# Kernel tuning notes

Hardware: AMD Instinct MI355X
Metric: run time of the kernel (lower is better)

Reference implementation:

```python
import jax, jax.numpy as jnp
import numpy as np

N_EMBD = 1024
N_HEAD = 16
HEAD_DIM = N_EMBD // N_HEAD  # 64
N_CTX = 2048
ROPE_THETA = 10000.0


def _rope_cache(L, dim, base):
    inv_freq = 1.0 / (base ** (np.arange(0, dim, 2, dtype=np.float32) / dim))
    t = np.arange(L, dtype=np.float32)
    freqs = np.einsum('i,j->ij', t, inv_freq)  # (L, dim/2)
    return jnp.asarray(np.cos(freqs)), jnp.asarray(np.sin(freqs))


def _apply_rotary(x, cos, sin):
    # x: (B, H, L, D), cos/sin: (L, D/2) -> broadcast (1,1,L,D/2)
    x1 = x[..., ::2]
    x2 = x[..., 1::2]
    c = cos[None, None, :, :]
    s = sin[None, None, :, :]
    y1 = x1 * c - x2 * s
    y2 = x1 * s + x2 * c
    # interleave back: stack on last dim then flatten
    return jnp.stack((y1, y2), axis=-1).reshape(x.shape)


def setup_inputs() -> dict:
    key = jax.random.key(0)
    k1, k2, k3, k4, k5 = jax.random.split(key, 5)
    B, L, D = 4, 2048, N_EMBD
    scale = 0.02
    x = jax.random.normal(k1, (B, L, D), dtype=jnp.float32)
    W_qkv = jax.random.normal(k2, (D, 3 * D), dtype=jnp.float32) * scale
    b_qkv = jnp.zeros((3 * D,), dtype=jnp.float32)
    W_proj = jax.random.normal(k3, (D, D), dtype=jnp.float32) * scale
    b_proj = jnp.zeros((D,), dtype=jnp.float32)
    attention_mask = jnp.ones((B, L), dtype=jnp.int32)
    return {"x": x, "W_qkv": W_qkv, "b_qkv": b_qkv, "W_proj": W_proj,
            "b_proj": b_proj, "attention_mask": attention_mask}


def reference(x, W_qkv, b_qkv, W_proj, b_proj, attention_mask):
    B, L, D = x.shape
    H, Dh = N_HEAD, HEAD_DIM
    qkv = x @ W_qkv + b_qkv  # (B, L, 3D)
    q, k, v = jnp.split(qkv, 3, axis=2)
    # (B, L, H, Dh) -> (B, H, L, Dh)
    q = q.reshape(B, L, H, Dh).transpose(0, 2, 1, 3)
    k = k.reshape(B, L, H, Dh).transpose(0, 2, 1, 3)
    v = v.reshape(B, L, H, Dh).transpose(0, 2, 1, 3)
    cos, sin = _rope_cache(L, Dh, ROPE_THETA)
    q = _apply_rotary(q, cos, sin)
    k = _apply_rotary(k, cos, sin)
    # mask: causal & key padding keep
    causal = jnp.tril(jnp.ones((L, L), dtype=bool))[None, None]        # (1,1,L,L)
    key_keep = attention_mask.astype(bool)[:, None, None, :]          # (B,1,1,L)
    keep = causal & key_keep                                          # (B,1,L,L)
    scores = jnp.einsum('bhqd,bhkd->bhqk', q, k) / jnp.sqrt(jnp.float32(Dh))
    scores = jnp.where(keep, scores, jnp.finfo(scores.dtype).min)
    attn = jax.nn.softmax(scores, axis=-1)
    out = jnp.einsum('bhqk,bhkd->bhqd', attn, v)  # (B,H,L,Dh)
    out = out.transpose(0, 2, 1, 3).reshape(B, L, D)
    return out @ W_proj + b_proj
```

## Files before the change

kernel.cpp:

```cpp
#include <hip/hip_runtime.h>
#include <math.h>

typedef __bf16 bf16x8 __attribute__((ext_vector_type(8)));
typedef float f32x4 __attribute__((ext_vector_type(4)));
typedef float f32x16 __attribute__((ext_vector_type(16)));
typedef unsigned short u16;
typedef unsigned short u16x8 __attribute__((ext_vector_type(8)));
typedef unsigned short u16x4 __attribute__((ext_vector_type(4)));
typedef unsigned u32x2v __attribute__((ext_vector_type(2)));

#define BATCH 4
#define SEQ   2048
#define EMBD  1024
#define NHEAD 16
#define HDIM  64
#define MROWS 8192
#define QKVN  3072

__device__ __forceinline__ u16 f2bf(float f) {
    union { float f; unsigned u; } cv; cv.f = f;
    unsigned u = cv.u;
    return (u16)((u + 0x7FFFu + ((u >> 16) & 1u)) >> 16);
}

__device__ __forceinline__ unsigned cvtpk_bf16(float lo, float hi) {
    unsigned r;
    asm("v_cvt_pk_bf16_f32 %0, %1, %2" : "=v"(r) : "v"(lo), "v"(hi));
    return r;
}

__device__ __forceinline__ void glds16(const void* g, void* l) {
    __builtin_amdgcn_global_load_lds(
        (const __attribute__((address_space(1))) unsigned int*)(g),
        (__attribute__((address_space(3))) unsigned int*)(l), 16, 0, 0);
}

#define MF8(qm, A0, A1, A2, A3, B0, B1)                                          \
    acc[(qm)*4+0][0] = __builtin_amdgcn_mfma_f32_16x16x32_bf16(A0, B0, acc[(qm)*4+0][0], 0, 0, 0); \
    acc[(qm)*4+0][1] = __builtin_amdgcn_mfma_f32_16x16x32_bf16(A0, B1, acc[(qm)*4+0][1], 0, 0, 0); \
    acc[(qm)*4+1][0] = __builtin_amdgcn_mfma_f32_16x16x32_bf16(A1, B0, acc[(qm)*4+1][0], 0, 0, 0); \
    acc[(qm)*4+1][1] = __builtin_amdgcn_mfma_f32_16x16x32_bf16(A1, B1, acc[(qm)*4+1][1], 0, 0, 0); \
    acc[(qm)*4+2][0] = __builtin_amdgcn_mfma_f32_16x16x32_bf16(A2, B0, acc[(qm)*4+2][0], 0, 0, 0); \
    acc[(qm)*4+2][1] = __builtin_amdgcn_mfma_f32_16x16x32_bf16(A2, B1, acc[(qm)*4+2][1], 0, 0, 0); \
    acc[(qm)*4+3][0] = __builtin_amdgcn_mfma_f32_16x16x32_bf16(A3, B0, acc[(qm)*4+3][0], 0, 0, 0); \
    acc[(qm)*4+3][1] = __builtin_amdgcn_mfma_f32_16x16x32_bf16(A3, B1, acc[(qm)*4+3][1], 0, 0, 0);

__device__ __forceinline__ void transpose_body(const float* __restrict__ W,
                                               u16* __restrict__ Wt, int K, int N,
                                               int n0, int k0, u16 (*T)[68]) {
    const int tx = threadIdx.x & 15, ty = threadIdx.x >> 4;
#pragma unroll
    for (int r = 0; r < 4; r++) {
        int k = k0 + ty + r * 16;
        float4 w = *(const float4*)&W[(size_t)k * N + n0 + tx * 4];
        T[tx * 4 + 0][ty + r * 16] = f2bf(w.x);
        T[tx * 4 + 1][ty + r * 16] = f2bf(w.y);
        T[tx * 4 + 2][ty + r * 16] = f2bf(w.z);
        T[tx * 4 + 3][ty + r * 16] = f2bf(w.w);
    }
    __syncthreads();
#pragma unroll
    for (int r = 0; r < 4; r++) {
        int nl = ty + r * 16;
        u16x4 v = { T[nl][tx * 4 + 0], T[nl][tx * 4 + 1],
                    T[nl][tx * 4 + 2], T[nl][tx * 4 + 3] };
        *(u16x4*)&Wt[(size_t)(n0 + nl) * K + k0 + tx * 4] = v;
    }
}

__global__ __launch_bounds__(256)
void prep_kernel(const float* __restrict__ x, const float* __restrict__ Wqkv,
                 const float* __restrict__ Wproj, const int* __restrict__ amask,
                 u16* __restrict__ Xb, u16* __restrict__ Wqkvt, u16* __restrict__ Wprojt,
                 float* __restrict__ ropeC, float* __restrict__ ropeS,
                 float* __restrict__ mbias, int* __restrict__ flags) {
    __shared__ union { u16 T[64][68]; int ok[4]; } sm;
    const int bx = blockIdx.x, tid = threadIdx.x;
    if (bx < 8192) {
        int i = bx * 256 + tid;
        float4 v = ((const float4*)x)[i];
        u16x4 o = { f2bf(v.x), f2bf(v.y), f2bf(v.z), f2bf(v.w) };
        ((u16x4*)Xb)[i] = o;
    } else if (bx < 8960) {
        int bxx = bx - 8192;
        transpose_body(Wqkv, Wqkvt, EMBD, QKVN, (bxx % 48) * 64, (bxx / 48) * 64, sm.T);
    } else if (bx < 9216) {
        int bxx = bx - 8960;
        transpose_body(Wproj, Wprojt, EMBD, EMBD, (bxx & 15) * 64, (bxx >> 4) * 64, sm.T);
    } else if (bx < 9472) {
        int i = (bx - 9216) * 256 + tid;
        int l = i >> 5, p = i & 31;
        float invf = powf(10000.0f, -(float)(2 * p) * (1.0f / 64.0f));
        float sv, cv;
        sincosf((float)l * invf, &sv, &cv);
        ropeC[i] = cv; ropeS[i] = sv;
    } else {
        int idx = (bx - 9472) * 256 + tid;
        int mv = amask[idx];
        mbias[idx] = mv ? 0.0f : -1e30f;
        unsigned long long bal = __ballot(mv != 0);
        int wv = tid >> 6;
        if ((tid & 63) == 0) sm.ok[wv] = (bal == 0xFFFFFFFFFFFFFFFFull);
        __syncthreads();
        if (tid == 0)   flags[idx >> 7] = sm.ok[0] & sm.ok[1];
        if (tid == 128) flags[idx >> 7] = sm.ok[2] & sm.ok[3];
    }
}

__global__ __launch_bounds__(512, 2)
void qkv_gemm(const u16* __restrict__ A, const u16* __restrict__ Bt,
              const float* __restrict__ bias,
              const float* __restrict__ Ct, const float* __restrict__ St,
              u16* __restrict__ Qo, u16* __restrict__ Ko, u16* __restrict__ Vo) {
    __shared__ u16 SM[49152];
    const int tid = threadIdx.x;
    const int w = tid >> 6, ln = tid & 63;
    const int quad = ln >> 4, l16 = ln & 15;
    const int wm = w >> 2, wn = w & 3;
    const int bid = blockIdx.y * 24 + blockIdx.x;
    const int swz = (bid & 7) * 96 + (bid >> 3);
    const int m0 = (swz / 24) * 256, n0 = (swz % 24) * 128;

    const int sr8 = ln >> 3;
    const int xs = (ln & 7) ^ sr8;
    const u16* Ab = A  + (size_t)(m0 + w * 8 + sr8) * EMBD + xs * 8;
    const u16* Bb = Bt + (size_t)(n0 + w * 8 + sr8) * EMBD + xs * 8;
    u16* ldsA = SM + w * 512;
    u16* ldsB = SM + 32768 + w * 512;
    const int ch0 = ((0 + quad) ^ (l16 & 7)) * 8;
    const int ch1 = ((4 + quad) ^ (l16 & 7)) * 8;

    auto stageA = [&](int buf, int rb, int kt) {
        glds16(Ab + (size_t)rb * EMBD + kt * 64, ldsA + buf * 16384 + rb * 64);
    };
    auto stageB = [&](int buf, int rb, int kt) {
        glds16(Bb + (size_t)rb * EMBD + kt * 64, ldsB + buf * 8192 + rb * 64);
    };

    f32x4 acc[8][2] = {};

    stageA(0, 0, 0);  stageA(0, 128, 0);
    stageA(0, 64, 0); stageA(0, 192, 0);
    stageB(0, 0, 0);  stageB(0, 64, 0);
    stageA(1, 0, 1);  stageA(1, 128, 1);
    asm volatile("s_waitcnt vmcnt(2)" ::: "memory");
    __builtin_amdgcn_sched_barrier(0);
    __builtin_amdgcn_s_barrier();

    for (int u = 0; u < 16; ++u) {
        const int c = u & 1, nc = c ^ 1;
        const u16* Ac0 = SM + c * 16384 + (wm * 128 + l16) * 64;
        const u16* Ac1 = Ac0 + 64 * 64;
        const u16* Bc  = SM + 32768 + c * 8192 + (wn * 32 + l16) * 64;
        bf16x8 a0, a1, a2, a3, bk0a, bk0b, bk1a, bk1b;
        a0 = *(const bf16x8*)&Ac0[ch0];        a1 = *(const bf16x8*)&Ac0[1024 + ch0];
        a2 = *(const bf16x8*)&Ac0[2048 + ch0]; a3 = *(const bf16x8*)&Ac0[3072 + ch0];
        bk0a = *(const bf16x8*)&Bc[ch0];       bk0b = *(const bf16x8*)&Bc[1024 + ch0];
        if (u < 15) { stageA(nc, 64, u + 1); stageA(nc, 192, u + 1); stageB(nc, 64, u + 1); }
        __builtin_amdgcn_sched_barrier(0);
        __builtin_amdgcn_s_setprio(1);
        MF8(0, a0, a1, a2, a3, bk0a, bk0b);
        __builtin_amdgcn_s_setprio(0);
        __builtin_amdgcn_sched_barrier(0);
        a0 = *(const bf16x8*)&Ac0[ch1];        a1 = *(const bf16x8*)&Ac0[1024 + ch1];
        a2 = *(const bf16x8*)&Ac0[2048 + ch1]; a3 = *(const bf16x8*)&Ac0[3072 + ch1];
        bk1a = *(const bf16x8*)&Bc[ch1];       bk1b = *(const bf16x8*)&Bc[1024 + ch1];
        if (u < 15) stageB(nc, 0, u + 1);
        __builtin_amdgcn_sched_barrier(0);
        __builtin_amdgcn_s_setprio(1);
        MF8(0, a0, a1, a2, a3, bk1a, bk1b);
        __builtin_amdgcn_s_setprio(0);
        __builtin_amdgcn_sched_barrier(0);
        __builtin_amdgcn_s_barrier();
        a0 = *(const bf16x8*)&Ac1[ch0];        a1 = *(const bf16x8*)&Ac1[1024 + ch0];
        a2 = *(const bf16x8*)&Ac1[2048 + ch0]; a3 = *(const bf16x8*)&Ac1[3072 + ch0];
        if (u < 14) { stageA(c, 0, u + 2); stageA(c, 128, u + 2); }
        __builtin_amdgcn_sched_barrier(0);
        __builtin_amdgcn_s_setprio(1);
        MF8(1, a0, a1, a2, a3, bk0a, bk0b);
        __builtin_amdgcn_s_setprio(0);
        __builtin_amdgcn_sched_barrier(0);
        a0 = *(const bf16x8*)&Ac1[ch1];        a1 = *(const bf16x8*)&Ac1[1024 + ch1];
        a2 = *(const bf16x8*)&Ac1[2048 + ch1]; a3 = *(const bf16x8*)&Ac1[3072 + ch1];
        __builtin_amdgcn_sched_barrier(0);
        __builtin_amdgcn_s_setprio(1);
        MF8(1, a0, a1, a2, a3, bk1a, bk1b);
        __builtin_amdgcn_s_setprio(0);
        __builtin_amdgcn_sched_barrier(0);
        if (u < 14) asm volatile("s_waitcnt vmcnt(2)" ::: "memory");
        else        asm volatile("s_waitcnt vmcnt(0)" ::: "memory");
        __builtin_amdgcn_sched_barrier(0);
        __builtin_amdgcn_s_barrier();
    }

    const int sec = n0 >> 10;
    if (sec == 2) {
#pragma unroll
        for (int ii = 0; ii < 8; ii++)
#pragma unroll
            for (int r = 0; r < 4; r++) {
                int m = m0 + wm * 128 + ii * 16 + quad * 4 + r;
                int b = m >> 11, l = m & 2047;
#pragma unroll
                for (int j = 0; j < 2; j++) {
                    int n = n0 + wn * 32 + j * 16 + l16;
                    int dcol = n & 1023;
                    int h = dcol >> 6, dh = dcol & 63;
                    float v = acc[ii][j][r] + bias[n];
                    Vo[(((size_t)b * NHEAD + h) * SEQ + l) * HDIM + dh] = f2bf(v);
                }
            }
    } else {
        u16* O = (sec == 0) ? Qo : Ko;
        const float qs = (sec == 0) ? 0.125f * 1.44269504f : 1.0f;
#pragma unroll
        for (int ii = 0; ii < 8; ii++)
#pragma unroll
            for (int r = 0; r < 4; r++) {
                int m = m0 + wm * 128 + ii * 16 + quad * 4 + r;
                int b = m >> 11, l = m & 2047;
#pragma unroll
                for (int j = 0; j < 2; j++) {
                    int n = n0 + wn * 32 + j * 16 + l16;
                    int h = (n & 1023) >> 6, dh = n & 63;
                    int p = (n & 63) >> 1;
                    float v = acc[ii][j][r] + bias[n];
                    float pv = __shfl_xor(v, 1, 64);
                    float cv = Ct[l * 32 + p], sv = St[l * 32 + p];
                    float o = (l16 & 1) ? (pv * sv + v * cv) : (v * cv - pv * sv);
                    O[(((size_t)b * NHEAD + h) * SEQ + l) * HDIM + dh] = f2bf(o * qs);
                }
            }
    }
}

__global__ __launch_bounds__(256)
void transpose_v(const u16* __restrict__ Vo, u16* __restrict__ Vt) {
    __shared__ u16 T[64][72];
    const int bh = blockIdx.y;
    const int l0 = blockIdx.x * 64;
    const int tx = threadIdx.x & 15, ty = threadIdx.x >> 4;
#pragma unroll
    for (int rr = 0; rr < 4; rr++) {
        int l = ty + rr * 16;
        u16x4 v = *(const u16x4*)&Vo[((size_t)bh * SEQ + l0 + l) * HDIM + tx * 4];
        T[l][tx * 4 + 0] = v.x; T[l][tx * 4 + 1] = v.y;
        T[l][tx * 4 + 2] = v.z; T[l][tx * 4 + 3] = v.w;
    }
    __syncthreads();
#pragma unroll
    for (int rr = 0; rr < 4; rr++) {
        int dh = ty + rr * 16;
        u16x4 w = { T[tx * 4 + 0][dh], T[tx * 4 + 1][dh],
                    T[tx * 4 + 2][dh], T[tx * 4 + 3][dh] };
        *(u16x4*)&Vt[((size_t)bh * HDIM + dh) * SEQ + l0 + tx * 4] = w;
    }
}

__global__ __launch_bounds__(512, 2)
void attn_mfma3(const u16* __restrict__ Qb, const u16* __restrict__ Kb,
                const u16* __restrict__ Vt, const float* __restrict__ mb,
                const int* __restrict__ flags, u16* __restrict__ Ot) {
    __shared__ u16 SM[32768];
    const int tid = threadIdx.x;
    const int wv = tid >> 6, ln = tid & 63;
    const int l32 = ln & 31, hi = ln >> 5;
    const int bid = blockIdx.x;
    const int bh = bid & 63;
    const int qt = (bid < 256) ? 7 - (bid >> 6) : ((bid - 256) >> 6);
    const int b = bh >> 4;
    const u16* Qg = Qb + (size_t)bh * SEQ * HDIM;
    const u16* Kg = Kb + (size_t)bh * SEQ * HDIM;
    const u16* Vg = Vt + (size_t)bh * HDIM * SEQ;

    const int kRow = ln >> 3;
    const size_t kLane = (size_t)(wv * 16 + kRow) * 64 + ((ln & 7) ^ kRow) * 8;
    const int vRow = ln >> 4, sc0 = (ln & 15) ^ vRow;
    const size_t vLaneE = (size_t)(wv * 8 + vRow) * SEQ + sc0 * 8;
    const size_t vLaneO = (size_t)(wv * 8 + 4 + vRow) * SEQ + (sc0 ^ 4) * 8;

    const int q0w = qt * 256 + wv * 32;
    const int qmin = q0w;
    const int qabs = q0w + l32;

    bf16x8 Qf[4];
#pragma unroll
    for (int kd = 0; kd < 4; kd++)
        Qf[kd] = *(const bf16x8*)&Qg[(size_t)(q0w + l32) * HDIM + kd * 16 + hi * 8];

    f32x16 o[2] = {};
    float mrun = -1e30f, lrun = 0.f;

    const int nkt = 2 * qt + 2;

    {
        u16* KsD = SM + wv * 1024;
        u16* VsD = SM + 8192 + wv * 1024;
        glds16(Kg + kLane,       KsD);
        glds16(Kg + kLane + 512, KsD + 512);
        glds16(Vg + vLaneE,      VsD);
        glds16(Vg + vLaneO,      VsD + 512);
    }
    __syncthreads();

    int buf = 0;
    for (int kt = 0; kt < nkt; kt++) {
        const int kbase = kt * 128;
        if (kt + 1 < nkt) {
            const size_t nb = (size_t)(kbase + 128);
            u16* KsD = SM + (buf ^ 1) * 16384 + wv * 1024;
            u16* VsD = SM + (buf ^ 1) * 16384 + 8192 + wv * 1024;
            glds16(Kg + nb * 64 + kLane,       KsD);
            glds16(Kg + nb * 64 + kLane + 512, KsD + 512);
            glds16(Vg + nb + vLaneE,           VsD);
            glds16(Vg + nb + vLaneO,           VsD + 512);
        }
        const u16* Ks = SM + buf * 16384;
        const u16* Vs = SM + buf * 16384 + 8192;

        f32x16 s[4];
        __builtin_amdgcn_s_setprio(1);
#pragma unroll
        for (int mi = 0; mi < 4; mi++) {
            const int key = mi * 32 + l32;
            f32x16 z = {};
#pragma unroll
            for (int kd = 0; kd < 4; kd++) {
                int ch = kd * 2 + hi;
                bf16x8 kf = *(const bf16x8*)&Ks[key * 64 + ((ch ^ (key & 7)) * 8)];
                z = __builtin_amdgcn_mfma_f32_32x32x16_bf16(kf, Qf[kd], z, 0, 0, 0);
            }
            s[mi] = z;
        }
        __builtin_amdgcn_s_setprio(0);

        if (kbase + 127 > qmin) {
#pragma unroll
            for (int mi = 0; mi < 4; mi++)
#pragma unroll
                for (int r = 0; r < 16; r++) {
                    int row = kbase + mi * 32 + (r & 3) + 8 * (r >> 2) + 4 * hi;
                    if (row > qabs) s[mi][r] = -1e30f;
                }
        }
        if (!flags[b * 16 + kt]) {
#pragma unroll
            for (int mi = 0; mi < 4; mi++)
#pragma unroll
                for (int r = 0; r < 16; r++) {
                    int row = mi * 32 + (r & 3) + 8 * (r >> 2) + 4 * hi;
                    s[mi][r] += mb[b * SEQ + kbase + row];
                }
        }

        float rm = -1e30f;
#pragma unroll
        for (int mi = 0; mi < 4; mi++) {
            float a0 = fmaxf(fmaxf(s[mi][0],  s[mi][1]),  fmaxf(s[mi][2],  s[mi][3]));
            float a1 = fmaxf(fmaxf(s[mi][4],  s[mi][5]),  fmaxf(s[mi][6],  s[mi][7]));
            float a2 = fmaxf(fmaxf(s[mi][8],  s[mi][9]),  fmaxf(s[mi][10], s[mi][11]));
            float a3 = fmaxf(fmaxf(s[mi][12], s[mi][13]), fmaxf(s[mi][14], s[mi][15]));
            rm = fmaxf(rm, fmaxf(fmaxf(a0, a1), fmaxf(a2, a3)));
        }
        {
            u32x2v f = __builtin_amdgcn_permlane32_swap(
                __float_as_uint(rm), __float_as_uint(rm), false, false);
            rm = fmaxf(__uint_as_float(f[0]), __uint_as_float(f[1]));
        }
        if (!__all(rm <= mrun + 8.0f)) {
            float mnew = fmaxf(mrun, rm);
            float al = __builtin_amdgcn_exp2f(mrun - mnew);
            mrun = mnew;
            lrun *= al;
#pragma unroll
            for (int r = 0; r < 16; r++) { o[0][r] *= al; o[1][r] *= al; }
        }
        float rs = 0.f;
#pragma unroll
        for (int mi = 0; mi < 4; mi++) {
            float ps = 0.f;
#pragma unroll
            for (int r = 0; r < 16; r++) {
                float pe = __builtin_amdgcn_exp2f(s[mi][r] - mrun);
                s[mi][r] = pe;
                ps += pe;
            }
            rs += ps;
        }
        {
            u32x2v f = __builtin_amdgcn_permlane32_swap(
                __float_as_uint(rs), __float_as_uint(rs), false, false);
            rs = __uint_as_float(f[0]) + __uint_as_float(f[1]);
        }
        lrun += rs;

#pragma unroll
        for (int t = 0; t < 4; t++) {
            unsigned A0 = cvtpk_bf16(s[t][0],  s[t][1]);
            unsigned B0 = cvtpk_bf16(s[t][4],  s[t][5]);
            unsigned A1 = cvtpk_bf16(s[t][2],  s[t][3]);
            unsigned B1 = cvtpk_bf16(s[t][6],  s[t][7]);
            u32x2v r0 = __builtin_amdgcn_permlane32_swap(A0, B0, false, false);
            u32x2v r1 = __builtin_amdgcn_permlane32_swap(A1, B1, false, false);
            union { unsigned u[4]; bf16x8 v; } p0;
            p0.u[0] = r0[0]; p0.u[1] = r1[0]; p0.u[2] = r0[1]; p0.u[3] = r1[1];

            unsigned A2 = cvtpk_bf16(s[t][8],  s[t][9]);
            unsigned B2 = cvtpk_bf16(s[t][12], s[t][13]);
            unsigned A3 = cvtpk_bf16(s[t][10], s[t][11]);
            unsigned B3 = cvtpk_bf16(s[t][14], s[t][15]);
            u32x2v r2 = __builtin_amdgcn_permlane32_swap(A2, B2, false, false);
            u32x2v r3 = __builtin_amdgcn_permlane32_swap(A3, B3, false, false);
            union { unsigned u[4]; bf16x8 v; } p1;
            p1.u[0] = r2[0]; p1.u[1] = r3[0]; p1.u[2] = r2[1]; p1.u[3] = r3[1];

            __builtin_amdgcn_s_setprio(1);
#pragma unroll
            for (int md = 0; md < 2; md++) {
                const int dh = md * 32 + l32;
                bf16x8 v0 = *(const bf16x8*)&Vs[dh * 128 + (((t * 4 + hi)     ^ (dh & 7)) * 8)];
                o[md] = __builtin_amdgcn_mfma_f32_32x32x16_bf16(v0, p0.v, o[md], 0, 0, 0);
                bf16x8 v1 = *(const bf16x8*)&Vs[dh * 128 + (((t * 4 + 2 + hi) ^ (dh & 7)) * 8)];
                o[md] = __builtin_amdgcn_mfma_f32_32x32x16_bf16(v1, p1.v, o[md], 0, 0, 0);
            }
            __builtin_amdgcn_s_setprio(0);
        }
        __syncthreads();
        buf ^= 1;
    }

    __syncthreads();
    u16* Osh = SM + wv * 2176;
    float inv = 1.0f / lrun;
#pragma unroll
    for (int md = 0; md < 2; md++)
#pragma unroll
        for (int r = 0; r < 16; r++) {
            int dh = md * 32 + (r & 3) + 8 * (r >> 2) + 4 * hi;
            Osh[l32 * 68 + dh] = f2bf(o[md][r] * inv);
        }
    __syncthreads();
    {
        int qrow = ln >> 1, hf = ln & 1;
        size_t gbase = ((size_t)bh * SEQ + q0w + qrow) * HDIM + hf * 32;
#pragma unroll
        for (int c = 0; c < 4; c++) {
            u16x8 vv = *(const u16x8*)&Osh[qrow * 68 + hf * 32 + c * 8];
            *(u16x8*)&Ot[gbase + c * 8] = vv;
        }
    }
}

__global__ __launch_bounds__(256)
void proj_gemm(const u16* __restrict__ A, const u16* __restrict__ Bt,
               const float* __restrict__ bias, float* __restrict__ out) {
    __shared__ u16 SM[32768];
    const int tid = threadIdx.x;
    const int wv = tid >> 6, ln = tid & 63;
    const int quad = ln >> 4, l16 = ln & 15;
    const int bid = blockIdx.y * 8 + blockIdx.x;
    const int swz = (bid & 7) * 64 + (bid >> 3);
    const int m0 = (swz >> 3) * 128, n0 = (swz & 7) * 128;
    const int wm = wv >> 1, wn = wv & 1;

    const int srow = wv * 8 + (ln >> 3);
    const int xs = (ln & 7) ^ (srow & 7);

    f32x4 acc[4][4] = {};

    auto stage = [&](int buf, int kt) {
        u16* As = SM + buf * 16384;
        u16* Bs = As + 8192;
#pragma unroll
        for (int p = 0; p < 4; p++) {
            int row = p * 32 + srow;
            int m = m0 + row;
            int bb = m >> 11, l = m & 2047;
            glds16(A + (((size_t)(bb * 16 + kt) * SEQ + l) * HDIM) + xs * 8,
                   As + (p * 256 + wv * 64) * 8);
            glds16(Bt + (size_t)(n0 + row) * EMBD + kt * 64 + xs * 8,
                   Bs + (p * 256 + wv * 64) * 8);
        }
    };

    stage(0, 0);
    __syncthreads();
    int buf = 0;
    for (int kt = 0; kt < 16; kt++) {
        if (kt < 15) stage(buf ^ 1, kt + 1);
        const u16* As = SM + buf * 16384;
        const u16* Bs = As + 8192;
        __builtin_amdgcn_s_setprio(1);
#pragma unroll
        for (int kk = 0; kk < 2; kk++) {
            bf16x8 af[4], bfr[4];
#pragma unroll
            for (int i = 0; i < 4; i++) {
                int R = wm * 64 + i * 16 + l16;
                af[i] = *(const bf16x8*)&As[R * 64 + (((kk * 4 + quad) ^ (R & 7)) * 8)];
            }
#pragma unroll
            for (int j = 0; j < 4; j++) {
                int R = wn * 64 + j * 16 + l16;
                bfr[j] = *(const bf16x8*)&Bs[R * 64 + (((kk * 4 + quad) ^ (R & 7)) * 8)];
            }
#pragma unroll
            for (int i = 0; i < 4; i++)
#pragma unroll
                for (int j = 0; j < 4; j++)
                    acc[i][j] = __builtin_amdgcn_mfma_f32_16x16x32_bf16(af[i], bfr[j], acc[i][j], 0, 0, 0);
        }
        __builtin_amdgcn_s_setprio(0);
        __syncthreads();
        buf ^= 1;
    }
#pragma unroll
    for (int i = 0; i < 4; i++)
#pragma unroll
        for (int r = 0; r < 4; r++) {
            int m = m0 + wm * 64 + i * 16 + quad * 4 + r;
#pragma unroll
            for (int j = 0; j < 4; j++) {
                int n = n0 + wn * 64 + j * 16 + l16;
                out[(size_t)m * EMBD + n] = acc[i][j][r] + bias[n];
            }
        }
}

extern "C" void kernel_launch(void* const* d_in, const int* in_sizes, int n_in,
                              void* d_out, int out_size, void* d_ws, size_t ws_size,
                              hipStream_t stream)
{
    const float* x     = (const float*)d_in[0];
    const float* Wqkv  = (const float*)d_in[1];
    const float* bqkv  = (const float*)d_in[2];
    const float* Wproj = (const float*)d_in[3];
    const float* bproj = (const float*)d_in[4];
    const int*   amask = (const int*)d_in[5];
    float* out = (float*)d_out;

    char* ws = (char*)d_ws;
    u16*   Xb     = (u16*)(ws);
    u16*   Ot     = (u16*)(ws);
    u16*   Wqkvt  = (u16*)(ws + 16777216);
    u16*   Wprojt = (u16*)(ws + 23068672);
    u16*   Qb     = (u16*)(ws + 25165824);
    u16*   Kb     = (u16*)(ws + 41943040);
    u16*   Vb     = (u16*)(ws + 58720256);
    u16*   Vtp    = (u16*)(ws + 75497472);
    float* ropeC  = (float*)(ws + 92274688);
    float* ropeS  = (float*)(ws + 92536832);
    float* mbias  = (float*)(ws + 92798976);
    int*   flags  = (int*)(ws + 92831744);

    prep_kernel<<<9504, 256, 0, stream>>>(x, Wqkv, Wproj, amask,
                                          Xb, Wqkvt, Wprojt, ropeC, ropeS, mbias, flags);
    qkv_gemm<<<dim3(24, 32), 512, 0, stream>>>(
        Xb, Wqkvt, bqkv, ropeC, ropeS, Qb, Kb, Vb);
    transpose_v<<<dim3(32, 64), 256, 0, stream>>>(Vb, Vtp);
    attn_mfma3<<<512, 512, 0, stream>>>(Qb, Kb, Vtp, mbias, flags, Ot);
    proj_gemm<<<dim3(EMBD / 128, MROWS / 128), 256, 0, stream>>>(Ot, Wprojt, bproj, out);
}
```

Baseline: 245.8 us.

## Fuse V transpose into QKV GEMM epilogue and skip fully masked causal tiles

The QKV GEMM's V-section epilogue now stages the tile in shared memory and writes V directly in the transposed (head, dim, seq) layout. This removes the separate transpose kernel and its extra round trip through global memory. In attention, each wave skips QK, softmax and PV work for key tiles that lie entirely above its causal diagonal. The cost is an extra LDS staging pass and a barrier in the GEMM epilogue, plus more branch divergence between waves in attention.

```diff
diff --git a/kernel.cpp b/kernel.cpp
--- a/kernel.cpp
+++ b/kernel.cpp
@@ -111,7 +111,7 @@
 void qkv_gemm(const u16* __restrict__ A, const u16* __restrict__ Bt,
               const float* __restrict__ bias,
               const float* __restrict__ Ct, const float* __restrict__ St,
-              u16* __restrict__ Qo, u16* __restrict__ Ko, u16* __restrict__ Vo) {
+              u16* __restrict__ Qo, u16* __restrict__ Ko, u16* __restrict__ Vt) {
     __shared__ u16 SM[49152];
     const int tid = threadIdx.x;
     const int w = tid >> 6, ln = tid & 63;
@@ -195,21 +195,33 @@
 
     const int sec = n0 >> 10;
     if (sec == 2) {
+        u16* Vl = SM;
 #pragma unroll
         for (int ii = 0; ii < 8; ii++)
 #pragma unroll
-            for (int r = 0; r < 4; r++) {
-                int m = m0 + wm * 128 + ii * 16 + quad * 4 + r;
-                int b = m >> 11, l = m & 2047;
-#pragma unroll
-                for (int j = 0; j < 2; j++) {
-                    int n = n0 + wn * 32 + j * 16 + l16;
-                    int dcol = n & 1023;
-                    int h = dcol >> 6, dh = dcol & 63;
-                    float v = acc[ii][j][r] + bias[n];
-                    Vo[(((size_t)b * NHEAD + h) * SEQ + l) * HDIM + dh] = f2bf(v);
-                }
-            }
+            for (int j = 0; j < 2; j++) {
+                int nl = wn * 32 + j * 16 + l16;
+                int ml = wm * 128 + ii * 16 + quad * 4;
+                int n = n0 + wn * 32 + j * 16 + l16;
+                u16x4 pk;
+#pragma unroll
+                for (int r = 0; r < 4; r++)
+                    pk[r] = f2bf(acc[ii][j][r] + bias[n]);
+                *(u16x4*)&Vl[nl * 260 + ml] = pk;
+            }
+        __syncthreads();
+        {
+            int dcl = tid >> 2, ck = tid & 3;
+            int dcol = (n0 & 1023) + dcl;
+            int h = dcol >> 6, dh = dcol & 63;
+            int b = m0 >> 11, l0 = m0 & 2047;
+            size_t gb = (((size_t)b * NHEAD + h) * HDIM + dh) * SEQ + l0 + ck * 64;
+#pragma unroll
+            for (int c2 = 0; c2 < 8; c2++) {
+                u16x8 v = *(const u16x8*)&Vl[dcl * 260 + ck * 64 + c2 * 8];
+                *(u16x8*)&Vt[gb + c2 * 8] = v;
+            }
+        }
     } else {
         u16* O = (sec == 0) ? Qo : Ko;
         const float qs = (sec == 0) ? 0.125f * 1.44269504f : 1.0f;
@@ -231,29 +243,6 @@
                     O[(((size_t)b * NHEAD + h) * SEQ + l) * HDIM + dh] = f2bf(o * qs);
                 }
             }
-    }
-}
-
-__global__ __launch_bounds__(256)
-void transpose_v(const u16* __restrict__ Vo, u16* __restrict__ Vt) {
-    __shared__ u16 T[64][72];
-    const int bh = blockIdx.y;
-    const int l0 = blockIdx.x * 64;
-    const int tx = threadIdx.x & 15, ty = threadIdx.x >> 4;
-#pragma unroll
-    for (int rr = 0; rr < 4; rr++) {
-        int l = ty + rr * 16;
-        u16x4 v = *(const u16x4*)&Vo[((size_t)bh * SEQ + l0 + l) * HDIM + tx * 4];
-        T[l][tx * 4 + 0] = v.x; T[l][tx * 4 + 1] = v.y;
-        T[l][tx * 4 + 2] = v.z; T[l][tx * 4 + 3] = v.w;
-    }
-    __syncthreads();
-#pragma unroll
-    for (int rr = 0; rr < 4; rr++) {
-        int dh = ty + rr * 16;
-        u16x4 w = { T[tx * 4 + 0][dh], T[tx * 4 + 1][dh],
-                    T[tx * 4 + 2][dh], T[tx * 4 + 3][dh] };
-        *(u16x4*)&Vt[((size_t)bh * HDIM + dh) * SEQ + l0 + tx * 4] = w;
     }
 }
 
@@ -280,7 +269,6 @@
     const size_t vLaneO = (size_t)(wv * 8 + 4 + vRow) * SEQ + (sc0 ^ 4) * 8;
 
     const int q0w = qt * 256 + wv * 32;
-    const int qmin = q0w;
     const int qabs = q0w + l32;
 
     bf16x8 Qf[4];
@@ -318,112 +306,114 @@
         const u16* Ks = SM + buf * 16384;
         const u16* Vs = SM + buf * 16384 + 8192;
 
-        f32x16 s[4];
-        __builtin_amdgcn_s_setprio(1);
-#pragma unroll
-        for (int mi = 0; mi < 4; mi++) {
-            const int key = mi * 32 + l32;
-            f32x16 z = {};
-#pragma unroll
-            for (int kd = 0; kd < 4; kd++) {
-                int ch = kd * 2 + hi;
-                bf16x8 kf = *(const bf16x8*)&Ks[key * 64 + ((ch ^ (key & 7)) * 8)];
-                z = __builtin_amdgcn_mfma_f32_32x32x16_bf16(kf, Qf[kd], z, 0, 0, 0);
-            }
-            s[mi] = z;
-        }
-        __builtin_amdgcn_s_setprio(0);
-
-        if (kbase + 127 > qmin) {
-#pragma unroll
-            for (int mi = 0; mi < 4; mi++)
+        if (kbase <= q0w + 31) {
+            f32x16 s[4];
+            __builtin_amdgcn_s_setprio(1);
+#pragma unroll
+            for (int mi = 0; mi < 4; mi++) {
+                const int key = mi * 32 + l32;
+                f32x16 z = {};
+#pragma unroll
+                for (int kd = 0; kd < 4; kd++) {
+                    int ch = kd * 2 + hi;
+                    bf16x8 kf = *(const bf16x8*)&Ks[key * 64 + ((ch ^ (key & 7)) * 8)];
+                    z = __builtin_amdgcn_mfma_f32_32x32x16_bf16(kf, Qf[kd], z, 0, 0, 0);
+                }
+                s[mi] = z;
+            }
+            __builtin_amdgcn_s_setprio(0);
+
+            if (kbase + 127 > q0w) {
+#pragma unroll
+                for (int mi = 0; mi < 4; mi++)
+#pragma unroll
+                    for (int r = 0; r < 16; r++) {
+                        int row = kbase + mi * 32 + (r & 3) + 8 * (r >> 2) + 4 * hi;
+                        if (row > qabs) s[mi][r] = -1e30f;
+                    }
+            }
+            if (!flags[b * 16 + kt]) {
+#pragma unroll
+                for (int mi = 0; mi < 4; mi++)
+#pragma unroll
+                    for (int r = 0; r < 16; r++) {
+                        int row = mi * 32 + (r & 3) + 8 * (r >> 2) + 4 * hi;
+                        s[mi][r] += mb[b * SEQ + kbase + row];
+                    }
+            }
+
+            float rm = -1e30f;
+#pragma unroll
+            for (int mi = 0; mi < 4; mi++) {
+                float a0 = fmaxf(fmaxf(s[mi][0],  s[mi][1]),  fmaxf(s[mi][2],  s[mi][3]));
+                float a1 = fmaxf(fmaxf(s[mi][4],  s[mi][5]),  fmaxf(s[mi][6],  s[mi][7]));
+                float a2 = fmaxf(fmaxf(s[mi][8],  s[mi][9]),  fmaxf(s[mi][10], s[mi][11]));
+                float a3 = fmaxf(fmaxf(s[mi][12], s[mi][13]), fmaxf(s[mi][14], s[mi][15]));
+                rm = fmaxf(rm, fmaxf(fmaxf(a0, a1), fmaxf(a2, a3)));
+            }
+            {
+                u32x2v f = __builtin_amdgcn_permlane32_swap(
+                    __float_as_uint(rm), __float_as_uint(rm), false, false);
+                rm = fmaxf(__uint_as_float(f[0]), __uint_as_float(f[1]));
+            }
+            if (!__all(rm <= mrun + 8.0f)) {
+                float mnew = fmaxf(mrun, rm);
+                float al = __builtin_amdgcn_exp2f(mrun - mnew);
+                mrun = mnew;
+                lrun *= al;
+#pragma unroll
+                for (int r = 0; r < 16; r++) { o[0][r] *= al; o[1][r] *= al; }
+            }
+            float rs = 0.f;
+#pragma unroll
+            for (int mi = 0; mi < 4; mi++) {
+                float ps = 0.f;
 #pragma unroll
                 for (int r = 0; r < 16; r++) {
-                    int row = kbase + mi * 32 + (r & 3) + 8 * (r >> 2) + 4 * hi;
-                    if (row > qabs) s[mi][r] = -1e30f;
+                    float pe = __builtin_amdgcn_exp2f(s[mi][r] - mrun);
+                    s[mi][r] = pe;
+                    ps += pe;
                 }
-        }
-        if (!flags[b * 16 + kt]) {
-#pragma unroll
-            for (int mi = 0; mi < 4; mi++)
-#pragma unroll
-                for (int r = 0; r < 16; r++) {
-                    int row = mi * 32 + (r & 3) + 8 * (r >> 2) + 4 * hi;
-                    s[mi][r] += mb[b * SEQ + kbase + row];
+                rs += ps;
+            }
+            {
+                u32x2v f = __builtin_amdgcn_permlane32_swap(
+                    __float_as_uint(rs), __float_as_uint(rs), false, false);
+                rs = __uint_as_float(f[0]) + __uint_as_float(f[1]);
+            }
+            lrun += rs;
+
+#pragma unroll
+            for (int t = 0; t < 4; t++) {
+                unsigned A0 = cvtpk_bf16(s[t][0],  s[t][1]);
+                unsigned B0 = cvtpk_bf16(s[t][4],  s[t][5]);
+                unsigned A1 = cvtpk_bf16(s[t][2],  s[t][3]);
+                unsigned B1 = cvtpk_bf16(s[t][6],  s[t][7]);
+                u32x2v r0 = __builtin_amdgcn_permlane32_swap(A0, B0, false, false);
+                u32x2v r1 = __builtin_amdgcn_permlane32_swap(A1, B1, false, false);
+                union { unsigned u[4]; bf16x8 v; } p0;
+                p0.u[0] = r0[0]; p0.u[1] = r1[0]; p0.u[2] = r0[1]; p0.u[3] = r1[1];
+
+                unsigned A2 = cvtpk_bf16(s[t][8],  s[t][9]);
+                unsigned B2 = cvtpk_bf16(s[t][12], s[t][13]);
+                unsigned A3 = cvtpk_bf16(s[t][10], s[t][11]);
+                unsigned B3 = cvtpk_bf16(s[t][14], s[t][15]);
+                u32x2v r2 = __builtin_amdgcn_permlane32_swap(A2, B2, false, false);
+                u32x2v r3 = __builtin_amdgcn_permlane32_swap(A3, B3, false, false);
+                union { unsigned u[4]; bf16x8 v; } p1;
+                p1.u[0] = r2[0]; p1.u[1] = r3[0]; p1.u[2] = r2[1]; p1.u[3] = r3[1];
+
+                __builtin_amdgcn_s_setprio(1);
+#pragma unroll
+                for (int md = 0; md < 2; md++) {
+                    const int dh = md * 32 + l32;
+                    bf16x8 v0 = *(const bf16x8*)&Vs[dh * 128 + (((t * 4 + hi)     ^ (dh & 7)) * 8)];
+                    o[md] = __builtin_amdgcn_mfma_f32_32x32x16_bf16(v0, p0.v, o[md], 0, 0, 0);
+                    bf16x8 v1 = *(const bf16x8*)&Vs[dh * 128 + (((t * 4 + 2 + hi) ^ (dh & 7)) * 8)];
+                    o[md] = __builtin_amdgcn_mfma_f32_32x32x16_bf16(v1, p1.v, o[md], 0, 0, 0);
                 }
-        }
-
-        float rm = -1e30f;
-#pragma unroll
-        for (int mi = 0; mi < 4; mi++) {
-            float a0 = fmaxf(fmaxf(s[mi][0],  s[mi][1]),  fmaxf(s[mi][2],  s[mi][3]));
-            float a1 = fmaxf(fmaxf(s[mi][4],  s[mi][5]),  fmaxf(s[mi][6],  s[mi][7]));
-            float a2 = fmaxf(fmaxf(s[mi][8],  s[mi][9]),  fmaxf(s[mi][10], s[mi][11]));
-            float a3 = fmaxf(fmaxf(s[mi][12], s[mi][13]), fmaxf(s[mi][14], s[mi][15]));
-            rm = fmaxf(rm, fmaxf(fmaxf(a0, a1), fmaxf(a2, a3)));
-        }
-        {
-            u32x2v f = __builtin_amdgcn_permlane32_swap(
-                __float_as_uint(rm), __float_as_uint(rm), false, false);
-            rm = fmaxf(__uint_as_float(f[0]), __uint_as_float(f[1]));
-        }
-        if (!__all(rm <= mrun + 8.0f)) {
-            float mnew = fmaxf(mrun, rm);
-            float al = __builtin_amdgcn_exp2f(mrun - mnew);
-            mrun = mnew;
-            lrun *= al;
-#pragma unroll
-            for (int r = 0; r < 16; r++) { o[0][r] *= al; o[1][r] *= al; }
-        }
-        float rs = 0.f;
-#pragma unroll
-        for (int mi = 0; mi < 4; mi++) {
-            float ps = 0.f;
-#pragma unroll
-            for (int r = 0; r < 16; r++) {
-                float pe = __builtin_amdgcn_exp2f(s[mi][r] - mrun);
-                s[mi][r] = pe;
-                ps += pe;
-            }
-            rs += ps;
-        }
-        {
-            u32x2v f = __builtin_amdgcn_permlane32_swap(
-                __float_as_uint(rs), __float_as_uint(rs), false, false);
-            rs = __uint_as_float(f[0]) + __uint_as_float(f[1]);
-        }
-        lrun += rs;
-
-#pragma unroll
-        for (int t = 0; t < 4; t++) {
-            unsigned A0 = cvtpk_bf16(s[t][0],  s[t][1]);
-            unsigned B0 = cvtpk_bf16(s[t][4],  s[t][5]);
-            unsigned A1 = cvtpk_bf16(s[t][2],  s[t][3]);
-            unsigned B1 = cvtpk_bf16(s[t][6],  s[t][7]);
-            u32x2v r0 = __builtin_amdgcn_permlane32_swap(A0, B0, false, false);
-            u32x2v r1 = __builtin_amdgcn_permlane32_swap(A1, B1, false, false);
-            union { unsigned u[4]; bf16x8 v; } p0;
-            p0.u[0] = r0[0]; p0.u[1] = r1[0]; p0.u[2] = r0[1]; p0.u[3] = r1[1];
-
-            unsigned A2 = cvtpk_bf16(s[t][8],  s[t][9]);
-            unsigned B2 = cvtpk_bf16(s[t][12], s[t][13]);
-            unsigned A3 = cvtpk_bf16(s[t][10], s[t][11]);
-            unsigned B3 = cvtpk_bf16(s[t][14], s[t][15]);
-            u32x2v r2 = __builtin_amdgcn_permlane32_swap(A2, B2, false, false);
-            u32x2v r3 = __builtin_amdgcn_permlane32_swap(A3, B3, false, false);
-            union { unsigned u[4]; bf16x8 v; } p1;
-            p1.u[0] = r2[0]; p1.u[1] = r3[0]; p1.u[2] = r2[1]; p1.u[3] = r3[1];
-
-            __builtin_amdgcn_s_setprio(1);
-#pragma unroll
-            for (int md = 0; md < 2; md++) {
-                const int dh = md * 32 + l32;
-                bf16x8 v0 = *(const bf16x8*)&Vs[dh * 128 + (((t * 4 + hi)     ^ (dh & 7)) * 8)];
-                o[md] = __builtin_amdgcn_mfma_f32_32x32x16_bf16(v0, p0.v, o[md], 0, 0, 0);
-                bf16x8 v1 = *(const bf16x8*)&Vs[dh * 128 + (((t * 4 + 2 + hi) ^ (dh & 7)) * 8)];
-                o[md] = __builtin_amdgcn_mfma_f32_32x32x16_bf16(v1, p1.v, o[md], 0, 0, 0);
-            }
-            __builtin_amdgcn_s_setprio(0);
+                __builtin_amdgcn_s_setprio(0);
+            }
         }
         __syncthreads();
         buf ^= 1;
@@ -546,7 +536,6 @@
     u16*   Wprojt = (u16*)(ws + 23068672);
     u16*   Qb     = (u16*)(ws + 25165824);
     u16*   Kb     = (u16*)(ws + 41943040);
-    u16*   Vb     = (u16*)(ws + 58720256);
     u16*   Vtp    = (u16*)(ws + 75497472);
     float* ropeC  = (float*)(ws + 92274688);
     float* ropeS  = (float*)(ws + 92536832);
@@ -556,8 +545,7 @@
     prep_kernel<<<9504, 256, 0, stream>>>(x, Wqkv, Wproj, amask,
                                           Xb, Wqkvt, Wprojt, ropeC, ropeS, mbias, flags);
     qkv_gemm<<<dim3(24, 32), 512, 0, stream>>>(
-        Xb, Wqkvt, bqkv, ropeC, ropeS, Qb, Kb, Vb);
-    transpose_v<<<dim3(32, 64), 256, 0, stream>>>(Vb, Vtp);
+        Xb, Wqkvt, bqkv, ropeC, ropeS, Qb, Kb, Vtp);
     attn_mfma3<<<512, 512, 0, stream>>>(Qb, Kb, Vtp, mbias, flags, Ot);
     proj_gemm<<<dim3(EMBD / 128, MROWS / 128), 256, 0, stream>>>(Ot, Wprojt, bproj, out);
 }
```

New measurement: 243.8 us. About the same (-0.8%).
